# Kernel tuning notes

Hardware: AMD Instinct MI355X
Metric: run time of the kernel (lower is better)

Reference implementation:

```python
import jax, jax.numpy as jnp
import numpy as np

LAMBDA_INIT = 0.8
EPS = 1e-5


def setup_inputs() -> dict:
    key = jax.random.key(0)
    k1, k2, k3, k4 = jax.random.split(key, 4)
    B, H, S, D = 2, 16, 2048, 64
    return {
        "query": jax.random.normal(k1, (B, H, S, D), dtype=jnp.float32),
        "key": jax.random.normal(k2, (B, H, S, D), dtype=jnp.float32),
        "value": jax.random.normal(k3, (B, H, S, D), dtype=jnp.float32),
        "lambda_params": jax.random.uniform(k4, (H,), dtype=jnp.float32),
    }


def reference(query, key, value, lambda_params):
    # query/key/value: [B, H, S, D]; lambda_params: [H]
    B, H, S, D = query.shape
    d2 = D // 2
    scale = 1.0 / jnp.sqrt(jnp.float32(d2))
    q1, q2 = query[..., :d2], query[..., d2:]
    k1, k2 = key[..., :d2], key[..., d2:]
    # Two softmax attention maps over the split halves: [B, H, Sq, Sk]
    a1 = jax.nn.softmax(jnp.einsum("bhqd,bhkd->bhqk", q1, k1) * scale, axis=-1)
    a2 = jax.nn.softmax(jnp.einsum("bhqd,bhkd->bhqk", q2, k2) * scale, axis=-1)
    lam = lambda_params[None, :, None, None]  # [1, H, 1, 1]
    attn = a1 - lam * a2
    out = jnp.einsum("bhqk,bhkd->bhqd", attn, value)  # [B, H, S, D]
    # Groupnorm-style normalization per (batch, head, position) over head_dim,
    # then rescale by (1 - lambda_init).
    mean = jnp.mean(out, axis=-1, keepdims=True)
    var = jnp.mean(jnp.square(out - mean), axis=-1, keepdims=True)
    out = (out - mean) * jax.lax.rsqrt(var + EPS)
    out = out * (1.0 - LAMBDA_INIT)
    return out
```

## Files before the change

kernel.cpp:

```cpp
#include <hip/hip_runtime.h>

typedef __bf16 bf16x8 __attribute__((ext_vector_type(8)));
typedef float f32x4 __attribute__((ext_vector_type(4)));

static __device__ __forceinline__ f32x4 mfma16(bf16x8 a, bf16x8 b, f32x4 c) {
  return __builtin_amdgcn_mfma_f32_16x16x32_bf16(a, b, c, 0, 0, 0);
}
static __device__ __forceinline__ unsigned cvtpk(float lo, float hi) {
  unsigned r;
  asm("v_cvt_pk_bf16_f32 %0, %1, %2" : "=v"(r) : "v"(lo), "v"(hi));
  return r;
}

__global__ __launch_bounds__(256)
void kpack(const float* __restrict__ K, __bf16* __restrict__ KS) {
  const int bh = blockIdx.x >> 6, ch = blockIdx.x & 63;
  const int t = threadIdx.x;
  const int t2 = t >> 7, br = (t >> 6) & 1, g = (t >> 4) & 3, c = t & 15;
  const float* src = K + ((size_t)bh * 2048 + ch * 32 + t2 * 16 + c) * 64 + br * 32 + g * 8;
  float4 f0 = *(const float4*)src;
  float4 f1 = *(const float4*)(src + 4);
  bf16x8 v;
  v[0] = (__bf16)f0.x; v[1] = (__bf16)f0.y; v[2] = (__bf16)f0.z; v[3] = (__bf16)f0.w;
  v[4] = (__bf16)f1.x; v[5] = (__bf16)f1.y; v[6] = (__bf16)f1.z; v[7] = (__bf16)f1.w;
  *(bf16x8*)(KS + (size_t)bh * 131072 + ch * 2048 + t * 8) = v;
}

__global__ __launch_bounds__(256)
void vpack(const float* __restrict__ V, __bf16* __restrict__ VS) {
  __shared__ float tile[64][65];
  const int bh = blockIdx.x >> 5;
  const int s0 = (blockIdx.x & 31) * 64;
  const int t = threadIdx.x;
  const float* Vb = V + (size_t)bh * 2048 * 64;
#pragma unroll
  for (int i = 0; i < 4; ++i) {
    const int r = i * 16 + (t >> 4);
    const int c4 = (t & 15) * 4;
    float4 v = *(const float4*)(Vb + (s0 + r) * 64 + c4);
    tile[r][c4] = v.x; tile[r][c4 + 1] = v.y;
    tile[r][c4 + 2] = v.z; tile[r][c4 + 3] = v.w;
  }
  __syncthreads();
  const int dt = t >> 6, g = (t >> 4) & 3, c = t & 15;
#pragma unroll
  for (int hh = 0; hh < 2; ++hh) {
    const int ch = (blockIdx.x & 31) * 2 + hh;
    bf16x8 v;
#pragma unroll
    for (int j = 0; j < 8; ++j) v[j] = (__bf16)tile[hh * 32 + 8 * g + j][16 * dt + c];
    *(bf16x8*)(VS + (size_t)bh * 131072 + ch * 2048 + dt * 512 + g * 128 + c * 8) = v;
  }
}

__global__ __launch_bounds__(256, 2)
void diffattn(const float* __restrict__ Q, const __bf16* __restrict__ KS,
              const __bf16* __restrict__ VS, const float* __restrict__ LP,
              float* __restrict__ OUT) {
  constexpr int S = 2048, D = 64;
  constexpr float QSCALE = 0.17677669529663687f * 1.4426950408889634f;

  __shared__ __align__(16) uint2 Pl[4][2][2][16][10];

  const int raw = blockIdx.x;
  const int wg  = (raw & 7) * 64 + (raw >> 3);
  const int bh  = wg >> 4;
  const int qb  = wg & 15;
  const float lam = LP[bh & 15];

  const int tid  = threadIdx.x;
  const int w    = tid >> 6;
  const int lane = tid & 63;
  const int c    = lane & 15;
  const int g    = lane >> 4;
  const int q0   = qb * 128 + w * 32;

  const float*  Qb    = Q  + (size_t)bh * S * D;
  const __bf16* Kbase = KS + (size_t)bh * 131072 + g * 128 + c * 8;
  const __bf16* Vbase = VS + (size_t)bh * 131072 + g * 128 + c * 8;

  bf16x8 aones;
  {
    uint4 u = make_uint4(0x3F803F80u, 0x3F803F80u, 0x3F803F80u, 0x3F803F80u);
    aones = __builtin_bit_cast(bf16x8, u);
  }

  bf16x8 bq[2][2];
#pragma unroll
  for (int qt = 0; qt < 2; ++qt)
#pragma unroll
    for (int br = 0; br < 2; ++br) {
      const float* p = Qb + (q0 + qt * 16 + c) * D + br * 32 + 8 * g;
      float4 f0 = *(const float4*)p;
      float4 f1 = *(const float4*)(p + 4);
      bf16x8 v;
      v[0] = (__bf16)(f0.x * QSCALE); v[1] = (__bf16)(f0.y * QSCALE);
      v[2] = (__bf16)(f0.z * QSCALE); v[3] = (__bf16)(f0.w * QSCALE);
      v[4] = (__bf16)(f1.x * QSCALE); v[5] = (__bf16)(f1.y * QSCALE);
      v[6] = (__bf16)(f1.z * QSCALE); v[7] = (__bf16)(f1.w * QSCALE);
      bq[qt][br] = v;
    }

  f32x4 acc[2][2][5];
#pragma unroll
  for (int qt = 0; qt < 2; ++qt)
#pragma unroll
    for (int br = 0; br < 2; ++br)
#pragma unroll
      for (int dt = 0; dt < 5; ++dt)
        acc[qt][br][dt] = (f32x4){0.f, 0.f, 0.f, 0.f};

#define LOADK(ak, ch) do {                                             \
    const __bf16* _p = Kbase + (size_t)(ch) * 2048;                    \
    ak[0][0] = *(const bf16x8*)_p;                                     \
    ak[0][1] = *(const bf16x8*)(_p + 512);                             \
    ak[1][0] = *(const bf16x8*)(_p + 1024);                            \
    ak[1][1] = *(const bf16x8*)(_p + 1536);                            \
  } while (0)

#define LOADV(av, ch) do {                                             \
    const __bf16* _p = Vbase + (size_t)(ch) * 2048;                    \
    _Pragma("unroll")                                                  \
    for (int dt = 0; dt < 4; ++dt)                                     \
      av[dt] = *(const bf16x8*)(_p + dt * 512);                        \
  } while (0)

#define STEP(akc, akn, avc, avn, ch) do {                                 \
    LOADK(akn, ((ch) + 1) & 63);                                          \
    LOADV(avn, ((ch) + 1) & 63);                                          \
     \
    _Pragma("unroll")                                                     \
    for (int qt = 0; qt < 2; ++qt)                                        \
      _Pragma("unroll")                                                   \
      for (int br = 0; br < 2; ++br) {                                    \
        f32x4 z = {0.f, 0.f, 0.f, 0.f};                                   \
        f32x4 sA = mfma16(akc[0][br], bq[qt][br], z);                     \
        f32x4 sB = mfma16(akc[1][br], bq[qt][br], z);                     \
        float pA[4], pB[4];                                               \
        _Pragma("unroll")                                                 \
        for (int r = 0; r < 4; ++r) {                                     \
          pA[r] = __builtin_amdgcn_exp2f(sA[r]);                          \
          pB[r] = __builtin_amdgcn_exp2f(sB[r]);                          \
        }                                                                 \
        uint2 uA; uA.x = cvtpk(pA[0], pA[1]); uA.y = cvtpk(pA[2], pA[3]); \
        uint2 uB; uB.x = cvtpk(pB[0], pB[1]); uB.y = cvtpk(pB[2], pB[3]); \
        Pl[w][qt][br][c][g]     = uA;                                     \
        Pl[w][qt][br][c][4 + g] = uB;                                     \
      }                                                                   \
    __builtin_amdgcn_sched_barrier(0);       \
             \
    _Pragma("unroll")                                                     \
    for (int qt = 0; qt < 2; ++qt)                                        \
      _Pragma("unroll")                                                   \
      for (int br = 0; br < 2; ++br) {                                    \
        uint2 lo = Pl[w][qt][br][c][2 * g];                               \
        uint2 hi = Pl[w][qt][br][c][2 * g + 1];                           \
        uint4 u = make_uint4(lo.x, lo.y, hi.x, hi.y);                     \
        bf16x8 bp = __builtin_bit_cast(bf16x8, u);                        \
        _Pragma("unroll")                                                 \
        for (int dt = 0; dt < 4; ++dt)                                    \
          acc[qt][br][dt] = mfma16(avc[dt], bp, acc[qt][br][dt]);         \
        acc[qt][br][4] = mfma16(aones, bp, acc[qt][br][4]);               \
      }                                                                   \
    __builtin_amdgcn_sched_barrier(0);   \
  } while (0)

  bf16x8 k0[2][2], k1[2][2], v0[4], v1[4];
  LOADK(k0, 0);
  LOADV(v0, 0);

#pragma unroll 1
  for (int ch = 0; ch < 64; ch += 2) {
    STEP(k0, k1, v0, v1, ch);
    STEP(k1, k0, v1, v0, ch + 1);
  }
#undef STEP
#undef LOADV
#undef LOADK

#pragma unroll
  for (int qt = 0; qt < 2; ++qt) {
    const float inv1 = 1.0f / acc[qt][0][4][0];
    const float inv2 = lam / acc[qt][1][4][0];

    float vals[16];
    float sum = 0.f, sq = 0.f;
#pragma unroll
    for (int dt = 0; dt < 4; ++dt)
#pragma unroll
      for (int r = 0; r < 4; ++r) {
        float x = acc[qt][0][dt][r] * inv1 - acc[qt][1][dt][r] * inv2;
        vals[dt * 4 + r] = x;
        sum += x; sq += x * x;
      }
    sum += __shfl_xor(sum, 16); sum += __shfl_xor(sum, 32);
    sq  += __shfl_xor(sq, 16);  sq  += __shfl_xor(sq, 32);
    const float mean = sum * (1.0f / 64.0f);
    const float var  = sq * (1.0f / 64.0f) - mean * mean;
    const float rstd = rsqrtf(var + 1e-5f) * 0.2f;

    float* op = OUT + (size_t)bh * S * D + (size_t)(q0 + qt * 16 + c) * D;
#pragma unroll
    for (int dt = 0; dt < 4; ++dt) {
      float4 o;
      o.x = (vals[dt * 4 + 0] - mean) * rstd;
      o.y = (vals[dt * 4 + 1] - mean) * rstd;
      o.z = (vals[dt * 4 + 2] - mean) * rstd;
      o.w = (vals[dt * 4 + 3] - mean) * rstd;
      *(float4*)(op + 16 * dt + 4 * g) = o;
    }
  }
}

extern "C" void kernel_launch(void* const* d_in, const int* in_sizes, int n_in,
                              void* d_out, int out_size, void* d_ws, size_t ws_size,
                              hipStream_t stream) {
  (void)in_sizes; (void)n_in; (void)out_size; (void)ws_size;
  const float* q  = (const float*)d_in[0];
  const float* k  = (const float*)d_in[1];
  const float* v  = (const float*)d_in[2];
  const float* lp = (const float*)d_in[3];
  float* out = (float*)d_out;

  __bf16* ks = (__bf16*)d_ws;
  __bf16* vs = (__bf16*)((char*)d_ws + (8u << 20));

  kpack<<<dim3(2048), dim3(256), 0, stream>>>(k, ks);
  vpack<<<dim3(1024), dim3(256), 0, stream>>>(v, vs);
  diffattn<<<dim3(512), dim3(256), 0, stream>>>(q, ks, vs, lp, out);
}
```

Measured before the change: 76.00 us.

## Switch attention MFMAs to 32x32x16 tiles and compute row sums on VALU

Replaces the 16x16x32 bf16 MFMA tiling with 32x32x16 MFMAs for both QK^T and PV, with the K/V pack layouts and the LDS staging of P reorganised to match. The softmax denominator is now summed in registers on the VALU instead of through an extra MFMA against a ones vector, which removes a fifth of the PV matrix work. Larger MFMA tiles cut instruction count and operand traffic, at the cost of 16-wide accumulators that raise register pressure, plus extra VALU adds per step.

```diff
diff --git a/kernel.cpp b/kernel.cpp
--- a/kernel.cpp
+++ b/kernel.cpp
@@ -1,10 +1,10 @@
 #include <hip/hip_runtime.h>
 
 typedef __bf16 bf16x8 __attribute__((ext_vector_type(8)));
-typedef float f32x4 __attribute__((ext_vector_type(4)));
-
-static __device__ __forceinline__ f32x4 mfma16(bf16x8 a, bf16x8 b, f32x4 c) {
-  return __builtin_amdgcn_mfma_f32_16x16x32_bf16(a, b, c, 0, 0, 0);
+typedef float f32x16 __attribute__((ext_vector_type(16)));
+
+static __device__ __forceinline__ f32x16 mfma32(bf16x8 a, bf16x8 b, f32x16 c) {
+  return __builtin_amdgcn_mfma_f32_32x32x16_bf16(a, b, c, 0, 0, 0);
 }
 static __device__ __forceinline__ unsigned cvtpk(float lo, float hi) {
   unsigned r;
@@ -16,8 +16,8 @@
 void kpack(const float* __restrict__ K, __bf16* __restrict__ KS) {
   const int bh = blockIdx.x >> 6, ch = blockIdx.x & 63;
   const int t = threadIdx.x;
-  const int t2 = t >> 7, br = (t >> 6) & 1, g = (t >> 4) & 3, c = t & 15;
-  const float* src = K + ((size_t)bh * 2048 + ch * 32 + t2 * 16 + c) * 64 + br * 32 + g * 8;
+  const int br = t >> 7, dc = (t >> 6) & 1, hi = (t >> 5) & 1, m = t & 31;
+  const float* src = K + ((size_t)bh * 2048 + ch * 32 + m) * 64 + br * 32 + dc * 16 + hi * 8;
   float4 f0 = *(const float4*)src;
   float4 f1 = *(const float4*)(src + 4);
   bf16x8 v;
@@ -42,14 +42,14 @@
     tile[r][c4 + 2] = v.z; tile[r][c4 + 3] = v.w;
   }
   __syncthreads();
-  const int dt = t >> 6, g = (t >> 4) & 3, c = t & 15;
+  const int dh = t >> 7, kc = (t >> 6) & 1, hi = (t >> 5) & 1, m = t & 31;
 #pragma unroll
   for (int hh = 0; hh < 2; ++hh) {
     const int ch = (blockIdx.x & 31) * 2 + hh;
     bf16x8 v;
 #pragma unroll
-    for (int j = 0; j < 8; ++j) v[j] = (__bf16)tile[hh * 32 + 8 * g + j][16 * dt + c];
-    *(bf16x8*)(VS + (size_t)bh * 131072 + ch * 2048 + dt * 512 + g * 128 + c * 8) = v;
+    for (int j = 0; j < 8; ++j) v[j] = (__bf16)tile[hh * 32 + kc * 16 + hi * 8 + j][dh * 32 + m];
+    *(bf16x8*)(VS + (size_t)bh * 131072 + ch * 2048 + t * 8) = v;
   }
 }
 
@@ -60,7 +60,7 @@
   constexpr int S = 2048, D = 64;
   constexpr float QSCALE = 0.17677669529663687f * 1.4426950408889634f;
 
-  __shared__ __align__(16) uint2 Pl[4][2][2][16][10];
+  __shared__ __align__(16) uint2 Pw[4][2][32][10];
 
   const int raw = blockIdx.x;
   const int wg  = (raw & 7) * 64 + (raw >> 3);
@@ -71,26 +71,20 @@
   const int tid  = threadIdx.x;
   const int w    = tid >> 6;
   const int lane = tid & 63;
-  const int c    = lane & 15;
-  const int g    = lane >> 4;
+  const int q    = lane & 31;
+  const int hi   = lane >> 5;
   const int q0   = qb * 128 + w * 32;
 
   const float*  Qb    = Q  + (size_t)bh * S * D;
-  const __bf16* Kbase = KS + (size_t)bh * 131072 + g * 128 + c * 8;
-  const __bf16* Vbase = VS + (size_t)bh * 131072 + g * 128 + c * 8;
-
-  bf16x8 aones;
-  {
-    uint4 u = make_uint4(0x3F803F80u, 0x3F803F80u, 0x3F803F80u, 0x3F803F80u);
-    aones = __builtin_bit_cast(bf16x8, u);
-  }
+  const __bf16* Kbase = KS + (size_t)bh * 131072 + lane * 8;
+  const __bf16* Vbase = VS + (size_t)bh * 131072 + lane * 8;
 
   bf16x8 bq[2][2];
 #pragma unroll
-  for (int qt = 0; qt < 2; ++qt)
-#pragma unroll
-    for (int br = 0; br < 2; ++br) {
-      const float* p = Qb + (q0 + qt * 16 + c) * D + br * 32 + 8 * g;
+  for (int br = 0; br < 2; ++br)
+#pragma unroll
+    for (int dc = 0; dc < 2; ++dc) {
+      const float* p = Qb + (size_t)(q0 + q) * D + br * 32 + dc * 16 + hi * 8;
       float4 f0 = *(const float4*)p;
       float4 f1 = *(const float4*)(p + 4);
       bf16x8 v;
@@ -98,17 +92,11 @@
       v[2] = (__bf16)(f0.z * QSCALE); v[3] = (__bf16)(f0.w * QSCALE);
       v[4] = (__bf16)(f1.x * QSCALE); v[5] = (__bf16)(f1.y * QSCALE);
       v[6] = (__bf16)(f1.z * QSCALE); v[7] = (__bf16)(f1.w * QSCALE);
-      bq[qt][br] = v;
+      bq[br][dc] = v;
     }
 
-  f32x4 acc[2][2][5];
-#pragma unroll
-  for (int qt = 0; qt < 2; ++qt)
-#pragma unroll
-    for (int br = 0; br < 2; ++br)
-#pragma unroll
-      for (int dt = 0; dt < 5; ++dt)
-        acc[qt][br][dt] = (f32x4){0.f, 0.f, 0.f, 0.f};
+  f32x16 acc[2][2] = {};
+  float rsum[2] = {0.f, 0.f};
 
 #define LOADK(ak, ch) do {                                             \
     const __bf16* _p = Kbase + (size_t)(ch) * 2048;                    \
@@ -120,52 +108,55 @@
 
 #define LOADV(av, ch) do {                                             \
     const __bf16* _p = Vbase + (size_t)(ch) * 2048;                    \
-    _Pragma("unroll")                                                  \
-    for (int dt = 0; dt < 4; ++dt)                                     \
-      av[dt] = *(const bf16x8*)(_p + dt * 512);                        \
+    av[0][0] = *(const bf16x8*)_p;                                     \
+    av[0][1] = *(const bf16x8*)(_p + 512);                             \
+    av[1][0] = *(const bf16x8*)(_p + 1024);                            \
+    av[1][1] = *(const bf16x8*)(_p + 1536);                            \
   } while (0)
 
-#define STEP(akc, akn, avc, avn, ch) do {                                 \
-    LOADK(akn, ((ch) + 1) & 63);                                          \
-    LOADV(avn, ((ch) + 1) & 63);                                          \
-     \
+#define STEP(kc_, kn_, vc_, vn_, ch) do {                                 \
+    LOADK(kn_, ((ch) + 1) & 63);                                          \
+    LOADV(vn_, ((ch) + 1) & 63);                                          \
+           \
     _Pragma("unroll")                                                     \
-    for (int qt = 0; qt < 2; ++qt)                                        \
+    for (int br = 0; br < 2; ++br) {                                      \
+      f32x16 z = {};                                                      \
+      f32x16 s = mfma32(kc_[br][1], bq[br][1],                            \
+                        mfma32(kc_[br][0], bq[br][0], z));                \
+      float p[16];                                                        \
       _Pragma("unroll")                                                   \
-      for (int br = 0; br < 2; ++br) {                                    \
-        f32x4 z = {0.f, 0.f, 0.f, 0.f};                                   \
-        f32x4 sA = mfma16(akc[0][br], bq[qt][br], z);                     \
-        f32x4 sB = mfma16(akc[1][br], bq[qt][br], z);                     \
-        float pA[4], pB[4];                                               \
-        _Pragma("unroll")                                                 \
-        for (int r = 0; r < 4; ++r) {                                     \
-          pA[r] = __builtin_amdgcn_exp2f(sA[r]);                          \
-          pB[r] = __builtin_amdgcn_exp2f(sB[r]);                          \
-        }                                                                 \
-        uint2 uA; uA.x = cvtpk(pA[0], pA[1]); uA.y = cvtpk(pA[2], pA[3]); \
-        uint2 uB; uB.x = cvtpk(pB[0], pB[1]); uB.y = cvtpk(pB[2], pB[3]); \
-        Pl[w][qt][br][c][g]     = uA;                                     \
-        Pl[w][qt][br][c][4 + g] = uB;                                     \
+      for (int r = 0; r < 16; ++r) p[r] = __builtin_amdgcn_exp2f(s[r]);   \
+      rsum[br] += ((p[0]+p[1])+(p[2]+p[3])) + ((p[4]+p[5])+(p[6]+p[7]))   \
+                + ((p[8]+p[9])+(p[10]+p[11])) + ((p[12]+p[13])+(p[14]+p[15])); \
+      unsigned u0 = cvtpk(p[0], p[1]),   u1 = cvtpk(p[2], p[3]);          \
+      unsigned u2 = cvtpk(p[4], p[5]),   u3 = cvtpk(p[6], p[7]);          \
+      unsigned u4 = cvtpk(p[8], p[9]),   u5 = cvtpk(p[10], p[11]);        \
+      unsigned u6 = cvtpk(p[12], p[13]), u7 = cvtpk(p[14], p[15]);        \
+      Pw[w][br][q][hi]     = make_uint2(u0, u1);     \
+      Pw[w][br][q][2 + hi] = make_uint2(u2, u3);     \
+      Pw[w][br][q][4 + hi] = make_uint2(u4, u5);     \
+      Pw[w][br][q][6 + hi] = make_uint2(u6, u7);     \
+    }                                                                     \
+    __builtin_amdgcn_sched_barrier(0);           \
+                           \
+    _Pragma("unroll")                                                     \
+    for (int br = 0; br < 2; ++br) {                                      \
+      uint2 a0 = Pw[w][br][q][2 * hi];               \
+      uint2 a1 = Pw[w][br][q][2 * hi + 1];           \
+      uint2 b0 = Pw[w][br][q][4 + 2 * hi];           \
+      uint2 b1 = Pw[w][br][q][5 + 2 * hi];                                \
+      bf16x8 bp0 = __builtin_bit_cast(bf16x8, make_uint4(a0.x, a0.y, a1.x, a1.y)); \
+      bf16x8 bp1 = __builtin_bit_cast(bf16x8, make_uint4(b0.x, b0.y, b1.x, b1.y)); \
+      _Pragma("unroll")                                                   \
+      for (int dh = 0; dh < 2; ++dh) {                                    \
+        acc[br][dh] = mfma32(vc_[dh][0], bp0, acc[br][dh]);               \
+        acc[br][dh] = mfma32(vc_[dh][1], bp1, acc[br][dh]);               \
       }                                                                   \
-    __builtin_amdgcn_sched_barrier(0);       \
-             \
-    _Pragma("unroll")                                                     \
-    for (int qt = 0; qt < 2; ++qt)                                        \
-      _Pragma("unroll")                                                   \
-      for (int br = 0; br < 2; ++br) {                                    \
-        uint2 lo = Pl[w][qt][br][c][2 * g];                               \
-        uint2 hi = Pl[w][qt][br][c][2 * g + 1];                           \
-        uint4 u = make_uint4(lo.x, lo.y, hi.x, hi.y);                     \
-        bf16x8 bp = __builtin_bit_cast(bf16x8, u);                        \
-        _Pragma("unroll")                                                 \
-        for (int dt = 0; dt < 4; ++dt)                                    \
-          acc[qt][br][dt] = mfma16(avc[dt], bp, acc[qt][br][dt]);         \
-        acc[qt][br][4] = mfma16(aones, bp, acc[qt][br][4]);               \
-      }                                                                   \
+    }                                                                     \
     __builtin_amdgcn_sched_barrier(0);   \
   } while (0)
 
-  bf16x8 k0[2][2], k1[2][2], v0[4], v1[4];
+  bf16x8 k0[2][2], k1[2][2], v0[2][2], v1[2][2];
   LOADK(k0, 0);
   LOADV(v0, 0);
 
@@ -178,38 +169,39 @@
 #undef LOADV
 #undef LOADK
 
-#pragma unroll
-  for (int qt = 0; qt < 2; ++qt) {
-    const float inv1 = 1.0f / acc[qt][0][4][0];
-    const float inv2 = lam / acc[qt][1][4][0];
-
-    float vals[16];
-    float sum = 0.f, sq = 0.f;
-#pragma unroll
-    for (int dt = 0; dt < 4; ++dt)
-#pragma unroll
-      for (int r = 0; r < 4; ++r) {
-        float x = acc[qt][0][dt][r] * inv1 - acc[qt][1][dt][r] * inv2;
-        vals[dt * 4 + r] = x;
-        sum += x; sq += x * x;
-      }
-    sum += __shfl_xor(sum, 16); sum += __shfl_xor(sum, 32);
-    sq  += __shfl_xor(sq, 16);  sq  += __shfl_xor(sq, 32);
-    const float mean = sum * (1.0f / 64.0f);
-    const float var  = sq * (1.0f / 64.0f) - mean * mean;
-    const float rstd = rsqrtf(var + 1e-5f) * 0.2f;
-
-    float* op = OUT + (size_t)bh * S * D + (size_t)(q0 + qt * 16 + c) * D;
-#pragma unroll
-    for (int dt = 0; dt < 4; ++dt) {
+  const float rs1 = rsum[0] + __shfl_xor(rsum[0], 32);
+  const float rs2 = rsum[1] + __shfl_xor(rsum[1], 32);
+  const float inv1 = 1.0f / rs1;
+  const float inv2 = lam / rs2;
+
+  float xv[2][16];
+  float sum = 0.f, sq = 0.f;
+#pragma unroll
+  for (int dh = 0; dh < 2; ++dh)
+#pragma unroll
+    for (int r = 0; r < 16; ++r) {
+      float x = acc[0][dh][r] * inv1 - acc[1][dh][r] * inv2;
+      xv[dh][r] = x;
+      sum += x; sq += x * x;
+    }
+  sum += __shfl_xor(sum, 32);
+  sq  += __shfl_xor(sq, 32);
+  const float mean = sum * (1.0f / 64.0f);
+  const float var  = sq * (1.0f / 64.0f) - mean * mean;
+  const float rstd = rsqrtf(var + 1e-5f) * 0.2f;
+
+  float* op = OUT + (size_t)bh * S * D + (size_t)(q0 + q) * D;
+#pragma unroll
+  for (int dh = 0; dh < 2; ++dh)
+#pragma unroll
+    for (int qd = 0; qd < 4; ++qd) {
       float4 o;
-      o.x = (vals[dt * 4 + 0] - mean) * rstd;
-      o.y = (vals[dt * 4 + 1] - mean) * rstd;
-      o.z = (vals[dt * 4 + 2] - mean) * rstd;
-      o.w = (vals[dt * 4 + 3] - mean) * rstd;
-      *(float4*)(op + 16 * dt + 4 * g) = o;
+      o.x = (xv[dh][4 * qd + 0] - mean) * rstd;
+      o.y = (xv[dh][4 * qd + 1] - mean) * rstd;
+      o.z = (xv[dh][4 * qd + 2] - mean) * rstd;
+      o.w = (xv[dh][4 * qd + 3] - mean) * rstd;
+      *(float4*)(op + 32 * dh + 8 * qd + 4 * hi) = o;
     }
-  }
 }
 
 extern "C" void kernel_launch(void* const* d_in, const int* in_sizes, int n_in,
```

After: 80.06 us. 1.05x slower.
